# Kernel tuning notes

Measured on AMD Instinct MI355X. Metric: run time of the kernel, lower is better.

The kernel has to match this reference:

```python
import jax, jax.numpy as jnp
import numpy as np

B_, L_, V = 256, 256, 44
DM, DI, DS, DR, NL = 256, 512, 16, 16, 6  # d_model, d_inner, d_state, dt_rank, n_layers
MLP_H = 128


def setup_inputs():
    key = jax.random.key(0)
    ks = jax.random.split(key, 16)
    def nrm(i, shape, s=0.02):
        return jax.random.normal(ks[i], shape, jnp.float32) * s
    tok = jax.random.randint(ks[0], (B_, L_), 0, V, dtype=jnp.int32)
    mask = jax.random.randint(ks[1], (B_, L_), 0, 2, dtype=jnp.int32)
    emb = nrm(2, (V, 64), 0.02)
    emb = emb.at[0].set(0.0)  # padding_idx=0
    conv_w = nrm(3, (DM, 64, 3), 0.05)
    bn_gamma = jnp.ones((DM,), jnp.float32)
    bn_beta = jnp.zeros((DM,), jnp.float32)
    in_proj_w = nrm(4, (NL, 2 * DI, DM))
    conv1d_w = nrm(5, (NL, DI, 4), 0.2)
    conv1d_b = jnp.zeros((NL, DI), jnp.float32)
    x_proj_w = nrm(6, (NL, DR + 2 * DS, DI))
    dt_proj_w = nrm(7, (NL, DI, DR), 0.1)
    dt_proj_b = -4.0 + nrm(8, (NL, DI), 0.5)
    A_log = jnp.log(jnp.arange(1, DS + 1, dtype=jnp.float32))[None, None, :] * jnp.ones((NL, DI, 1), jnp.float32)
    Dp = jnp.ones((NL, DI), jnp.float32)
    out_proj_w = nrm(9, (NL, DM, DI))
    norm1_w = jnp.ones((NL, DM), jnp.float32)
    norm2_w = jnp.ones((NL, DM), jnp.float32)
    fc1_w = nrm(10, (NL, 2 * MLP_H, DM))
    fc2_w = nrm(11, (NL, DM, MLP_H))
    normf_w = jnp.ones((DM,), jnp.float32)
    normf_b = jnp.zeros((DM,), jnp.float32)
    bind_w = nrm(12, (3, DM))
    bind_b = jnp.zeros((3,), jnp.float32)
    return {"smiles_token_id": tok, "smiles_token_mask": mask, "emb": emb, "conv_w": conv_w,
            "bn_gamma": bn_gamma, "bn_beta": bn_beta, "in_proj_w": in_proj_w, "conv1d_w": conv1d_w,
            "conv1d_b": conv1d_b, "x_proj_w": x_proj_w, "dt_proj_w": dt_proj_w, "dt_proj_b": dt_proj_b,
            "A_log": A_log, "Dp": Dp, "out_proj_w": out_proj_w, "norm1_w": norm1_w, "norm2_w": norm2_w,
            "fc1_w": fc1_w, "fc2_w": fc2_w, "normf_w": normf_w, "normf_b": normf_b,
            "bind_w": bind_w, "bind_b": bind_b}


def rmsnorm(x, w, eps=1e-4):
    return x * jax.lax.rsqrt(jnp.mean(x * x, -1, keepdims=True) + eps) * w


def layernorm(x, w, b, eps=1e-4):
    mu = jnp.mean(x, -1, keepdims=True)
    var = jnp.mean((x - mu) ** 2, -1, keepdims=True)
    return (x - mu) * jax.lax.rsqrt(var + eps) * w + b


def mamba1(x, inw, cw, cb, xpw, dtw, dtb, Alog, D, outw):
    # x: [B,L,DM]
    B, L, _ = x.shape
    xz = x @ inw.T                                   # [B,L,2*DI]
    xi, z = jnp.split(xz, 2, axis=-1)
    # depthwise causal conv1d, kernel 4 (torch pads 3 then truncates to L)
    xp = jnp.pad(xi, ((0, 0), (3, 0), (0, 0)))
    xc = cb + sum(cw[:, k] * xp[:, k:k + L, :] for k in range(4))
    xc = jax.nn.silu(xc)                             # [B,L,DI]
    xdbl = xc @ xpw.T                                # [B,L,DR+2*DS]
    dt = xdbl[..., :DR]
    Bm = xdbl[..., DR:DR + DS]                       # [B,L,DS]
    Cm = xdbl[..., DR + DS:]
    dt = jax.nn.softplus(dt @ dtw.T + dtb)           # [B,L,DI]
    A = -jnp.exp(Alog)                               # [DI,DS]

    def step(h, inp):
        dt_t, u_t, B_t, C_t = inp                    # [B,DI],[B,DI],[B,DS],[B,DS]
        dA = jnp.exp(dt_t[:, :, None] * A)           # [B,DI,DS]
        h = dA * h + (dt_t * u_t)[:, :, None] * B_t[:, None, :]
        y = jnp.einsum('bdn,bn->bd', h, C_t)
        return h, y

    h0 = jnp.zeros((B, DI, DS), x.dtype)
    xs = (dt.transpose(1, 0, 2), xc.transpose(1, 0, 2), Bm.transpose(1, 0, 2), Cm.transpose(1, 0, 2))
    _, ys = jax.lax.scan(step, h0, xs)               # [L,B,DI]
    y = ys.transpose(1, 0, 2) + xc * D
    y = y * jax.nn.silu(z)
    return y @ outw.T                                # [B,L,DM]


def _forward(tok, mask, emb, conv_w, bn_gamma, bn_beta, in_proj_w, conv1d_w, conv1d_b,
             x_proj_w, dt_proj_w, dt_proj_b, A_log, Dp, out_proj_w, norm1_w, norm2_w,
             fc1_w, fc2_w, normf_w, normf_b, bind_w, bind_b):
    B, L = tok.shape
    x = emb[tok]                                     # [B,L,64]
    # conv embedding 64->256, k=3, pad=1 + BN(eval: mean 0, var 1, eps=1e-3) + relu
    xp = jnp.pad(x, ((0, 0), (1, 0 + 1), (0, 0)))
    y = sum(jnp.einsum('bli,oi->blo', xp[:, k:k + L, :], conv_w[:, :, k]) for k in range(3))
    y = y * (bn_gamma * jax.lax.rsqrt(jnp.float32(1.0 + 1e-3))) + bn_beta
    hidden = jax.nn.relu(y)                          # [B,L,DM]
    residual = None
    for i in range(NL):
        residual = hidden if residual is None else hidden + residual
        hs = rmsnorm(residual, norm1_w[i])
        hs = mamba1(hs, in_proj_w[i], conv1d_w[i], conv1d_b[i], x_proj_w[i],
                    dt_proj_w[i], dt_proj_b[i], A_log[i], Dp[i], out_proj_w[i])
        residual = hs + residual
        hs = rmsnorm(residual, norm2_w[i])
        yg = hs @ fc1_w[i].T                          # [B,L,2*MLP_H]
        y_, g = jnp.split(yg, 2, axis=-1)
        hidden = (y_ * jax.nn.silu(g)) @ fc2_w[i].T   # GatedMLP
        # dropout p=0.1 is identity in eval
    zf = layernorm(hidden + residual, normf_w, normf_b)
    m = mask[..., None].astype(jnp.float32)
    pool = (zf * m).sum(1) / m.sum(1)
    bind = pool @ bind_w.T + bind_b
    return jax.nn.sigmoid(bind)                       # [B,3]


def reference(smiles_token_id, smiles_token_mask, emb, conv_w, bn_gamma, bn_beta, in_proj_w,
              conv1d_w, conv1d_b, x_proj_w, dt_proj_w, dt_proj_b, A_log, Dp, out_proj_w,
              norm1_w, norm2_w, fc1_w, fc2_w, normf_w, normf_b, bind_w, bind_b):
    return _forward(smiles_token_id, smiles_token_mask, emb, conv_w, bn_gamma, bn_beta,
                    in_proj_w, conv1d_w, conv1d_b, x_proj_w, dt_proj_w, dt_proj_b, A_log, Dp,
                    out_proj_w, norm1_w, norm2_w, fc1_w, fc2_w, normf_w, normf_b, bind_w, bind_b)
```

## Files before the change

kernel.cpp:

```cpp
#include <hip/hip_runtime.h>
#include <math.h>

#define B_TOT 256
#define L_SEQ 256
#define DM 256
#define DI 512
#define DS 16
#define NL 6
#define MLPH 128
#define ED 64

typedef unsigned short u16;
typedef unsigned int   u32;
using bf16x8 = __attribute__((ext_vector_type(8))) short;
using f32x4  = __attribute__((ext_vector_type(4))) float;

__device__ __forceinline__ float f_sigmoid(float x){ return 1.f/(1.f+__expf(-x)); }
__device__ __forceinline__ float f_silu(float x){ return x/(1.f+__expf(-x)); }
__device__ __forceinline__ u16 f2bf(float x){
  union { float f; u32 u; } v; v.f = x;
  u32 r = v.u + 0x7fffu + ((v.u >> 16) & 1u);
  return (u16)(r >> 16);
}
__device__ __forceinline__ float bf2f(u16 h){
  union { u32 u; float f; } v; v.u = ((u32)h) << 16; return v.f;
}
__device__ __forceinline__ void pow16(float p, float* pw){
  pw[0]=p; pw[1]=p*p; pw[2]=pw[0]*pw[1]; pw[3]=pw[1]*pw[1];
  pw[4]=pw[0]*pw[3]; pw[5]=pw[1]*pw[3]; pw[6]=pw[2]*pw[3]; pw[7]=pw[3]*pw[3];
  #pragma unroll
  for(int i=0;i<8;i++) pw[8+i]=pw[7]*pw[i];
}

__global__ __launch_bounds__(256) void k_cvt(const float* __restrict__ s, u16* __restrict__ d, int n){
  int i = blockIdx.x*256 + threadIdx.x;
  if (i < n) d[i] = f2bf(s[i]);
}
__global__ __launch_bounds__(256) void k_cvt_xproj(const float* __restrict__ s, u16* __restrict__ d){
  int i = blockIdx.x*256 + threadIdx.x;
  int k = i & 511; int n = (i>>9) & 63; int l = i >> 15;
  d[i] = (n < 48) ? f2bf(s[((size_t)l*48 + n)*512 + k]) : (u16)0;
}

__global__ __launch_bounds__(256) void k_embed_conv(
    const int* __restrict__ tok, const float* __restrict__ emb,
    const float* __restrict__ cw, const float* __restrict__ gamma,
    const float* __restrict__ beta, float* __restrict__ out)
{
  const int b  = blockIdx.y;
  const int lt = blockIdx.x;
  const int tid = threadIdx.x;
  __shared__ float xs[18][ED];
  for (int idx = tid; idx < 18*ED; idx += 256){
    int t = idx / ED, i = idx - t*ED;
    int l = lt*16 + t - 1;
    float v = 0.f;
    if (l >= 0 && l < L_SEQ) v = emb[tok[b*L_SEQ + l]*ED + i];
    xs[t][i] = v;
  }
  __syncthreads();
  const float g  = gamma[tid] * rsqrtf(1.001f);
  const float bt = beta[tid];
  const float* w = cw + (size_t)tid*(ED*3);
  float acc[16];
  #pragma unroll
  for (int t=0;t<16;t++) acc[t]=0.f;
  for (int i=0;i<ED;i++){
    float w0 = w[i*3+0], w1 = w[i*3+1], w2 = w[i*3+2];
    #pragma unroll
    for (int t=0;t<16;t++)
      acc[t] += xs[t][i]*w0 + xs[t+1][i]*w1 + xs[t+2][i]*w2;
  }
  #pragma unroll
  for (int t=0;t<16;t++){
    float v = acc[t]*g + bt;
    out[((size_t)(b*L_SEQ + lt*16 + t))*DM + tid] = fmaxf(v, 0.f);
  }
}

__global__ __launch_bounds__(256) void k_rms_first(
    const float* __restrict__ residual, const float* __restrict__ w, u16* __restrict__ out)
{
  const int row  = blockIdx.x*4 + (threadIdx.x >> 6);
  const int lane = threadIdx.x & 63;
  const size_t base = (size_t)row*DM;
  float4 v = ((const float4*)(residual + base))[lane];
  float ss = v.x*v.x + v.y*v.y + v.z*v.z + v.w*v.w;
  #pragma unroll
  for (int m=1; m<64; m<<=1) ss += __shfl_xor(ss, m);
  const float sc = rsqrtf(ss*(1.f/DM) + 1e-4f);
  float4 wv = ((const float4*)w)[lane];
  u32 p0 = f2bf(v.x*sc*wv.x) | ((u32)f2bf(v.y*sc*wv.y) << 16);
  u32 p1 = f2bf(v.z*sc*wv.z) | ((u32)f2bf(v.w*sc*wv.w) << 16);
  uint2 pk; pk.x = p0; pk.y = p1;
  *(uint2*)(out + base + lane*4) = pk;
}

__global__ __launch_bounds__(256) void k_final_ln(
    const float* __restrict__ x,
    const float* __restrict__ w, const float* __restrict__ bb, float* __restrict__ out)
{
  const int row  = blockIdx.x*4 + (threadIdx.x >> 6);
  const int lane = threadIdx.x & 63;
  const size_t base = (size_t)row*DM;
  float4 v = ((const float4*)(x + base))[lane];
  float s = v.x + v.y + v.z + v.w;
  #pragma unroll
  for (int m=1; m<64; m<<=1) s += __shfl_xor(s, m);
  const float mu = s*(1.f/DM);
  float4 c; c.x=v.x-mu; c.y=v.y-mu; c.z=v.z-mu; c.w=v.w-mu;
  float ss = c.x*c.x + c.y*c.y + c.z*c.z + c.w*c.w;
  #pragma unroll
  for (int m=1; m<64; m<<=1) ss += __shfl_xor(ss, m);
  const float sc = rsqrtf(ss*(1.f/DM) + 1e-4f);
  float4 wv = ((const float4*)w)[lane];
  float4 bv = ((const float4*)bb)[lane];
  float4 o;
  o.x = c.x*sc*wv.x + bv.x; o.y = c.y*sc*wv.y + bv.y;
  o.z = c.z*sc*wv.z + bv.z; o.w = c.w*sc*wv.w + bv.w;
  ((float4*)(out + base))[lane] = o;
}

template<int BN, bool BF16OUT>
__global__ __launch_bounds__(256) void k_gemm_bf(
    const u16* __restrict__ A, const u16* __restrict__ W,
    void* __restrict__ Cv, int Nc, int K)
{
  const int n0 = blockIdx.x * BN;
  const int m0 = blockIdx.y * 128;
  const int tid = threadIdx.x;
  const int w  = tid >> 6, l = tid & 63;
  const int wr = w >> 1, wc = w & 1;
  const int lr = l & 15, kb = l >> 4;
  constexpr int NJ = BN / 32;
  __shared__ uint4 As4[128*8];
  __shared__ uint4 Bs4[BN*8];
  f32x4 acc[4][NJ];
  #pragma unroll
  for (int i=0;i<4;i++)
    #pragma unroll
    for (int j=0;j<NJ;j++)
      acc[i][j] = (f32x4){0.f,0.f,0.f,0.f};
  const int srow = tid >> 3, schunk = tid & 7;
  for (int k0 = 0; k0 < K; k0 += 64){
    #pragma unroll
    for (int i=0;i<4;i++){
      int r = i*32 + srow;
      uint4 v = *(const uint4*)(A + (size_t)(m0 + r)*K + k0 + schunk*8);
      As4[r*8 + (schunk ^ (r & 7))] = v;
    }
    #pragma unroll
    for (int i=0;i<BN/32;i++){
      int r = i*32 + srow;
      uint4 v = *(const uint4*)(W + (size_t)(n0 + r)*K + k0 + schunk*8);
      Bs4[r*8 + (schunk ^ (r & 7))] = v;
    }
    __syncthreads();
    #pragma unroll
    for (int kk=0;kk<2;kk++){
      bf16x8 af[4], bfr[NJ];
      #pragma unroll
      for (int mi=0;mi<4;mi++){
        int r = wr*64 + mi*16 + lr;
        af[mi] = *(const bf16x8*)&As4[r*8 + ((kk*4 + kb) ^ (r & 7))];
      }
      #pragma unroll
      for (int ni=0;ni<NJ;ni++){
        int r = wc*(BN/2) + ni*16 + lr;
        bfr[ni] = *(const bf16x8*)&Bs4[r*8 + ((kk*4 + kb) ^ (r & 7))];
      }
      #pragma unroll
      for (int mi=0;mi<4;mi++)
        #pragma unroll
        for (int ni=0;ni<NJ;ni++)
          acc[mi][ni] = __builtin_amdgcn_mfma_f32_16x16x32_bf16(af[mi], bfr[ni], acc[mi][ni], 0, 0, 0);
    }
    __syncthreads();
  }
  #pragma unroll
  for (int mi=0;mi<4;mi++){
    #pragma unroll
    for (int ni=0;ni<NJ;ni++){
      int col = n0 + wc*(BN/2) + ni*16 + lr;
      if (col < Nc){
        #pragma unroll
        for (int r=0;r<4;r++){
          size_t row = (size_t)(m0 + wr*64 + mi*16 + kb*4 + r);
          if (BF16OUT) ((u16*)Cv)[row*Nc + col] = f2bf(acc[mi][ni][r]);
          else         ((float*)Cv)[row*Nc + col] = acc[mi][ni][r];
        }
      }
    }
  }
}

template<bool WRITE_HS>
__global__ __launch_bounds__(512) void k_gemm_rms(
    const u16* __restrict__ A, const u16* __restrict__ W,
    float* __restrict__ residual, const float* __restrict__ nw,
    u16* __restrict__ hs, int K)
{
  const int m0 = blockIdx.x * 128;
  const int tid = threadIdx.x;
  const int w = tid >> 6, l = tid & 63;
  const int wr = w >> 1, wc = w & 1;
  const int lr = l & 15, kb = l >> 4;
  __shared__ uint4 As4[128*8];
  __shared__ uint4 Bs4[256*8];
  __shared__ float red[128][2];
  f32x4 acc[2][8];
  #pragma unroll
  for (int i=0;i<2;i++)
    #pragma unroll
    for (int j=0;j<8;j++) acc[i][j] = (f32x4){0.f,0.f,0.f,0.f};
  const int srow = tid >> 3, schunk = tid & 7;
  for (int k0 = 0; k0 < K; k0 += 64){
    #pragma unroll
    for (int i=0;i<2;i++){
      int r = i*64 + srow;
      uint4 v = *(const uint4*)(A + (size_t)(m0 + r)*K + k0 + schunk*8);
      As4[r*8 + (schunk ^ (r & 7))] = v;
    }
    #pragma unroll
    for (int i=0;i<4;i++){
      int r = i*64 + srow;
      uint4 v = *(const uint4*)(W + (size_t)r*K + k0 + schunk*8);
      Bs4[r*8 + (schunk ^ (r & 7))] = v;
    }
    __syncthreads();
    #pragma unroll
    for (int kk=0;kk<2;kk++){
      bf16x8 af[2], bfr[8];
      #pragma unroll
      for (int mi=0;mi<2;mi++){
        int r = wr*32 + mi*16 + lr;
        af[mi] = *(const bf16x8*)&As4[r*8 + ((kk*4 + kb) ^ (r & 7))];
      }
      #pragma unroll
      for (int ni=0;ni<8;ni++){
        int r = wc*128 + ni*16 + lr;
        bfr[ni] = *(const bf16x8*)&Bs4[r*8 + ((kk*4 + kb) ^ (r & 7))];
      }
      #pragma unroll
      for (int mi=0;mi<2;mi++)
        #pragma unroll
        for (int ni=0;ni<8;ni++)
          acc[mi][ni] = __builtin_amdgcn_mfma_f32_16x16x32_bf16(af[mi], bfr[ni], acc[mi][ni], 0, 0, 0);
    }
    __syncthreads();
  }
  float p[2][4];
  #pragma unroll
  for (int mi=0;mi<2;mi++)
    #pragma unroll
    for (int r=0;r<4;r++) p[mi][r] = 0.f;
  #pragma unroll
  for (int mi=0;mi<2;mi++){
    #pragma unroll
    for (int ni=0;ni<8;ni++){
      int col = wc*128 + ni*16 + lr;
      #pragma unroll
      for (int r=0;r<4;r++){
        int row = wr*32 + mi*16 + kb*4 + r;
        float v = acc[mi][ni][r] + residual[(size_t)(m0+row)*DM + col];
        acc[mi][ni][r] = v;
        p[mi][r] += v*v;
      }
    }
  }
  #pragma unroll
  for (int mi=0;mi<2;mi++)
    #pragma unroll
    for (int r=0;r<4;r++){
      float s = p[mi][r];
      s += __shfl_xor(s, 1); s += __shfl_xor(s, 2);
      s += __shfl_xor(s, 4); s += __shfl_xor(s, 8);
      p[mi][r] = s;
    }
  if (lr == 0){
    #pragma unroll
    for (int mi=0;mi<2;mi++)
      #pragma unroll
      for (int r=0;r<4;r++)
        red[wr*32 + mi*16 + kb*4 + r][wc] = p[mi][r];
  }
  __syncthreads();
  #pragma unroll
  for (int mi=0;mi<2;mi++){
    float scm[4];
    #pragma unroll
    for (int r=0;r<4;r++){
      int row = wr*32 + mi*16 + kb*4 + r;
      scm[r] = rsqrtf((red[row][0]+red[row][1])*(1.f/DM) + 1e-4f);
    }
    #pragma unroll
    for (int ni=0;ni<8;ni++){
      int col = wc*128 + ni*16 + lr;
      float wn = WRITE_HS ? nw[col] : 0.f;
      #pragma unroll
      for (int r=0;r<4;r++){
        int row = wr*32 + mi*16 + kb*4 + r;
        float v = acc[mi][ni][r];
        residual[(size_t)(m0+row)*DM + col] = v;
        if (WRITE_HS) hs[(size_t)(m0+row)*DM + col] = f2bf(v*scm[r]*wn);
      }
    }
  }
}

__global__ __launch_bounds__(512) void k_fc1_glu(
    const u16* __restrict__ A, const u16* __restrict__ W, u16* __restrict__ out)
{
  const int K = DM;
  const int m0 = blockIdx.x * 128;
  const int tid = threadIdx.x;
  const int w = tid >> 6, l = tid & 63;
  const int wr = w >> 1, wc = w & 1;
  const int lr = l & 15, kb = l >> 4;
  __shared__ uint4 As4[128*8];
  __shared__ uint4 Bs4[256*8];
  f32x4 acc[2][8];
  #pragma unroll
  for (int i=0;i<2;i++)
    #pragma unroll
    for (int j=0;j<8;j++) acc[i][j] = (f32x4){0.f,0.f,0.f,0.f};
  const int srow = tid >> 3, schunk = tid & 7;
  for (int k0 = 0; k0 < K; k0 += 64){
    #pragma unroll
    for (int i=0;i<2;i++){
      int r = i*64 + srow;
      uint4 v = *(const uint4*)(A + (size_t)(m0 + r)*K + k0 + schunk*8);
      As4[r*8 + (schunk ^ (r & 7))] = v;
    }
    #pragma unroll
    for (int i=0;i<4;i++){
      int r = i*64 + srow;
      uint4 v = *(const uint4*)(W + (size_t)r*K + k0 + schunk*8);
      Bs4[r*8 + (schunk ^ (r & 7))] = v;
    }
    __syncthreads();
    #pragma unroll
    for (int kk=0;kk<2;kk++){
      bf16x8 af[2], bfr[8];
      #pragma unroll
      for (int mi=0;mi<2;mi++){
        int r = wr*32 + mi*16 + lr;
        af[mi] = *(const bf16x8*)&As4[r*8 + ((kk*4 + kb) ^ (r & 7))];
      }
      #pragma unroll
      for (int ni=0;ni<8;ni++){
        int r = (ni < 4) ? (wc*64 + ni*16 + lr) : (128 + wc*64 + (ni-4)*16 + lr);
        bfr[ni] = *(const bf16x8*)&Bs4[r*8 + ((kk*4 + kb) ^ (r & 7))];
      }
      #pragma unroll
      for (int mi=0;mi<2;mi++)
        #pragma unroll
        for (int ni=0;ni<8;ni++)
          acc[mi][ni] = __builtin_amdgcn_mfma_f32_16x16x32_bf16(af[mi], bfr[ni], acc[mi][ni], 0, 0, 0);
    }
    __syncthreads();
  }
  #pragma unroll
  for (int mi=0;mi<2;mi++){
    #pragma unroll
    for (int ni=0;ni<4;ni++){
      int jcol = wc*64 + ni*16 + lr;
      #pragma unroll
      for (int r=0;r<4;r++){
        int row = wr*32 + mi*16 + kb*4 + r;
        float y = acc[mi][ni][r];
        float g = acc[mi][ni+4][r];
        out[(size_t)(m0+row)*MLPH + jcol] = f2bf(y * f_silu(g));
      }
    }
  }
}

__global__ __launch_bounds__(256) void k_conv1d_silu(
    const u16* __restrict__ xz, const float* __restrict__ cw,
    const float* __restrict__ cb, u16* __restrict__ xcb)
{
  const int idx = blockIdx.x*256 + threadIdx.x;
  const int d0 = (idx & 63) * 8;
  const int m  = idx >> 6;
  const int l  = m & (L_SEQ-1);
  float acc[8];
  #pragma unroll
  for (int j=0;j<8;j++) acc[j] = cb[d0+j];
  float4 wv[8];
  #pragma unroll
  for (int j=0;j<8;j++) wv[j] = *(const float4*)(cw + (d0+j)*4);
  #pragma unroll
  for (int t=0;t<4;t++){
    if (l >= 3-t){
      bf16x8 v = *(const bf16x8*)(xz + (size_t)(m-3+t)*1024 + d0);
      #pragma unroll
      for (int j=0;j<8;j++){
        float wj = (t==0)?wv[j].x:(t==1)?wv[j].y:(t==2)?wv[j].z:wv[j].w;
        acc[j] += wj * bf2f((u16)v[j]);
      }
    }
  }
  u16 o[8];
  #pragma unroll
  for (int j=0;j<8;j++) o[j] = f2bf(f_silu(acc[j]));
  *(uint4*)(xcb + (size_t)m*DI + d0) = *(uint4*)o;
}

__global__ __launch_bounds__(512) void k_scan2(
    const float* __restrict__ xdbl, const u16* __restrict__ xcb,
    const u16* __restrict__ xz, u16* __restrict__ ybf,
    const float* __restrict__ A_log, const float* __restrict__ Dp,
    const float* __restrict__ dtw, const float* __restrict__ dtb)
{
  const int b = blockIdx.x;
  const int lane = threadIdx.x & 63;
  const int w = threadIdx.x >> 6;
  const int d = blockIdx.y*64 + lane;
  __shared__ __align__(16) float BD[L_SEQ][48];
  __shared__ __align__(16) float HE[8][64][20];
  __shared__ float SD[8][64];
  const size_t rowbase = (size_t)b*L_SEQ;
  {
    const float4* src = (const float4*)(xdbl + rowbase*48);
    float4* dst = (float4*)&BD[0][0];
    #pragma unroll
    for (int j=0;j<6;j++) dst[threadIdx.x + j*512] = src[threadIdx.x + j*512];
  }
  float dtw_r[16];
  #pragma unroll
  for (int k=0;k<16;k++) dtw_r[k] = dtw[(size_t)d*16 + k];
  const float dtb_r = dtb[d];
  bool structured = true;
  #pragma unroll
  for (int n=0;n<16;n++){
    float Ar = -__expf(A_log[(size_t)d*16 + n]);
    structured = structured && (fabsf(Ar + (float)(n+1)) < 1e-4f*(float)(n+1));
  }
  const float Dv = Dp[d];
  const int l0 = w*32;
  float u_cur[8], z_cur[8];
  #pragma unroll
  for (int s=0;s<8;s++){
    u_cur[s] = bf2f(xcb[(rowbase+l0+s)*DI + d]);
    z_cur[s] = bf2f(xz [(rowbase+l0+s)*1024 + 512 + d]);
  }
  __syncthreads();
  float h[16];
  #pragma unroll
  for (int n=0;n<16;n++) h[n]=0.f;
  float cum = 0.f;
  float cumdt[32], silz[32];
  #pragma unroll
  for (int t8=0; t8<4; ++t8){
    float u_nxt[8], z_nxt[8];
    if (t8 < 3){
      #pragma unroll
      for (int s=0;s<8;s++){
        u_nxt[s] = bf2f(xcb[(rowbase+l0+t8*8+8+s)*DI + d]);
        z_nxt[s] = bf2f(xz [(rowbase+l0+t8*8+8+s)*1024 + 512 + d]);
      }
    }
    #pragma unroll
    for (int s=0;s<8;s++){
      const int i = t8*8 + s;
      const int l = l0 + i;
      const float u_v = u_cur[s], z_v = z_cur[s];
      const float4* bd4 = (const float4*)&BD[l][0];
      float4 x0=bd4[0], x1=bd4[1], x2=bd4[2], x3=bd4[3];
      float4 B0=bd4[4], B1=bd4[5], B2=bd4[6], B3=bd4[7];
      float4 C0=bd4[8], C1=bd4[9], C2=bd4[10], C3=bd4[11];
      float a0 = x0.x*dtw_r[0] + x1.x*dtw_r[4] + x2.x*dtw_r[8]  + x3.x*dtw_r[12];
      float a1 = x0.y*dtw_r[1] + x1.y*dtw_r[5] + x2.y*dtw_r[9]  + x3.y*dtw_r[13];
      float a2 = x0.z*dtw_r[2] + x1.z*dtw_r[6] + x2.z*dtw_r[10] + x3.z*dtw_r[14];
      float a3 = x0.w*dtw_r[3] + x1.w*dtw_r[7] + x2.w*dtw_r[11] + x3.w*dtw_r[15];
      const float xr = dtb_r + (a0+a1) + (a2+a3);
      const float ex = __expf(xr);
      const float dt_v = (xr > 20.f) ? xr : __logf(1.f + ex);
      cum += dt_v; cumdt[i] = cum;
      const float dtu = dt_v * u_v;
      float Bv[16] = {B0.x,B0.y,B0.z,B0.w,B1.x,B1.y,B1.z,B1.w,
                      B2.x,B2.y,B2.z,B2.w,B3.x,B3.y,B3.z,B3.w};
      float Cv[16] = {C0.x,C0.y,C0.z,C0.w,C1.x,C1.y,C1.z,C1.w,
                      C2.x,C2.y,C2.z,C2.w,C3.x,C3.y,C3.z,C3.w};
      float y0=0.f,y1=0.f,y2=0.f,y3=0.f;
      if (structured){
        const float p = 1.f/(1.f + ex);
        float pw[16]; pow16(p, pw);
        #pragma unroll
        for (int n=0;n<16;n++){
          h[n] = pw[n]*h[n] + dtu*Bv[n];
          float t = h[n]*Cv[n];
          if ((n&3)==0) y0 += t; else if ((n&3)==1) y1 += t;
          else if ((n&3)==2) y2 += t; else y3 += t;
        }
      } else {
        #pragma unroll
        for (int n=0;n<16;n++){
          float Ar = -__expf(A_log[(size_t)d*16 + n]);
          h[n] = __expf(dt_v*Ar)*h[n] + dtu*Bv[n];
          float t = h[n]*Cv[n];
          if ((n&3)==0) y0 += t; else if ((n&3)==1) y1 += t;
          else if ((n&3)==2) y2 += t; else y3 += t;
        }
      }
      const float sz = f_silu(z_v);
      silz[i] = sz;
      ybf[(rowbase+l)*DI + d] = f2bf((((y0+y1)+(y2+y3)) + u_v*Dv) * sz);
    }
    if (t8 < 3){
      #pragma unroll
      for (int s=0;s<8;s++){ u_cur[s]=u_nxt[s]; z_cur[s]=z_nxt[s]; }
    }
  }
  SD[w][lane] = cum;
  *(float4*)&HE[w][lane][0]  = make_float4(h[0],h[1],h[2],h[3]);
  *(float4*)&HE[w][lane][4]  = make_float4(h[4],h[5],h[6],h[7]);
  *(float4*)&HE[w][lane][8]  = make_float4(h[8],h[9],h[10],h[11]);
  *(float4*)&HE[w][lane][12] = make_float4(h[12],h[13],h[14],h[15]);
  __syncthreads();
  if (w == 0) return;
  float H0[16];
  #pragma unroll
  for (int n=0;n<16;n++) H0[n]=0.f;
  for (int c=0; c<w; ++c){
    float sdt = SD[c][lane];
    float4 e0 = *(const float4*)&HE[c][lane][0];
    float4 e1 = *(const float4*)&HE[c][lane][4];
    float4 e2 = *(const float4*)&HE[c][lane][8];
    float4 e3 = *(const float4*)&HE[c][lane][12];
    float he[16] = {e0.x,e0.y,e0.z,e0.w,e1.x,e1.y,e1.z,e1.w,
                    e2.x,e2.y,e2.z,e2.w,e3.x,e3.y,e3.z,e3.w};
    if (structured){
      float q = __expf(-sdt);
      float qw[16]; pow16(q, qw);
      #pragma unroll
      for (int n=0;n<16;n++) H0[n] = H0[n]*qw[n] + he[n];
    } else {
      #pragma unroll
      for (int n=0;n<16;n++){
        float Ar = -__expf(A_log[(size_t)d*16 + n]);
        H0[n] = H0[n]*__expf(Ar*sdt) + he[n];
      }
    }
  }
  #pragma unroll
  for (int t8=0; t8<4; ++t8){
    #pragma unroll
    for (int s=0;s<8;s++){
      const int i = t8*8 + s;
      const int l = l0 + i;
      const float4* bd4 = (const float4*)&BD[l][0];
      float4 C0=bd4[8], C1=bd4[9], C2=bd4[10], C3=bd4[11];
      float Cv[16] = {C0.x,C0.y,C0.z,C0.w,C1.x,C1.y,C1.z,C1.w,
                      C2.x,C2.y,C2.z,C2.w,C3.x,C3.y,C3.z,C3.w};
      float c0=0.f,c1=0.f,c2=0.f,c3=0.f;
      if (structured){
        float q = __expf(-cumdt[i]);
        float qw[16]; pow16(q, qw);
        #pragma unroll
        for (int n=0;n<16;n++){
          float t = Cv[n]*qw[n]*H0[n];
          if ((n&3)==0) c0 += t; else if ((n&3)==1) c1 += t;
          else if ((n&3)==2) c2 += t; else c3 += t;
        }
      } else {
        #pragma unroll
        for (int n=0;n<16;n++){
          float Ar = -__expf(A_log[(size_t)d*16 + n]);
          float t = Cv[n]*__expf(Ar*cumdt[i])*H0[n];
          if ((n&3)==0) c0 += t; else if ((n&3)==1) c1 += t;
          else if ((n&3)==2) c2 += t; else c3 += t;
        }
      }
      const float corr = (c0+c1)+(c2+c3);
      const size_t off = (rowbase+l)*DI + d;
      float prev = bf2f(ybf[off]);
      ybf[off] = f2bf(prev + corr*silz[i]);
    }
  }
}

__global__ __launch_bounds__(256) void k_pool(
    const float* __restrict__ zf, const int* __restrict__ mask,
    float* __restrict__ pool, int b0)
{
  const int b = blockIdx.x;
  const int d = threadIdx.x;
  __shared__ float mrow[L_SEQ];
  for (int l = d; l < L_SEQ; l += 256) mrow[l] = (float)mask[(size_t)(b0+b)*L_SEQ + l];
  __syncthreads();
  float s = 0.f, ms = 0.f;
  for (int l=0;l<L_SEQ;l++){
    float mv = mrow[l];
    s  += mv * zf[((size_t)b*L_SEQ + l)*DM + d];
    ms += mv;
  }
  pool[(size_t)(b0+b)*DM + d] = s/ms;
}

__global__ __launch_bounds__(64) void k_bind(
    const float* __restrict__ pool, const float* __restrict__ bw,
    const float* __restrict__ bb, float* __restrict__ out)
{
  const int b = blockIdx.x;
  const int lane = threadIdx.x;
  float4 p = ((const float4*)(pool + (size_t)b*DM))[lane];
  #pragma unroll
  for (int j=0;j<3;j++){
    float4 w = ((const float4*)(bw + (size_t)j*DM))[lane];
    float s = p.x*w.x + p.y*w.y + p.z*w.z + p.w*w.w;
    #pragma unroll
    for (int m=1;m<64;m<<=1) s += __shfl_xor(s, m);
    if (lane==0) out[b*3 + j] = f_sigmoid(s + bb[j]);
  }
}

extern "C" void kernel_launch(void* const* d_in, const int* in_sizes, int n_in,
                              void* d_out, int out_size, void* d_ws, size_t ws_size,
                              hipStream_t stream)
{
  const int*   tok       = (const int*)  d_in[0];
  const int*   mask      = (const int*)  d_in[1];
  const float* emb       = (const float*)d_in[2];
  const float* conv_w    = (const float*)d_in[3];
  const float* bn_gamma  = (const float*)d_in[4];
  const float* bn_beta   = (const float*)d_in[5];
  const float* in_proj_w = (const float*)d_in[6];
  const float* conv1d_w  = (const float*)d_in[7];
  const float* conv1d_b  = (const float*)d_in[8];
  const float* x_proj_w  = (const float*)d_in[9];
  const float* dt_proj_w = (const float*)d_in[10];
  const float* dt_proj_b = (const float*)d_in[11];
  const float* A_log     = (const float*)d_in[12];
  const float* Dp        = (const float*)d_in[13];
  const float* out_proj_w= (const float*)d_in[14];
  const float* norm1_w   = (const float*)d_in[15];
  const float* norm2_w   = (const float*)d_in[16];
  const float* fc1_w     = (const float*)d_in[17];
  const float* fc2_w     = (const float*)d_in[18];
  const float* normf_w   = (const float*)d_in[19];
  const float* normf_b   = (const float*)d_in[20];
  const float* bind_w    = (const float*)d_in[21];
  const float* bind_b    = (const float*)d_in[22];
  float* outp = (float*)d_out;

  char* base = (char*)d_ws;
  size_t off = 0;
  const int NIN = NL*2*DI*DM, NOUT = NL*DM*DI, NF1 = NL*2*MLPH*DM, NF2 = NL*DM*MLPH, NXP = NL*64*DI;
  u16* w_in  = (u16*)(base + off); off += (size_t)NIN*2;
  u16* w_out = (u16*)(base + off); off += (size_t)NOUT*2;
  u16* w_f1  = (u16*)(base + off); off += (size_t)NF1*2;
  u16* w_f2  = (u16*)(base + off); off += (size_t)NF2*2;
  u16* w_xp  = (u16*)(base + off); off += (size_t)NXP*2;
  float* pool = (float*)(base + off); off += (size_t)B_TOT*DM*4;
  const size_t fixed = off;

  const size_t perRow = 1216 + 4864;
  int Bc = B_TOT;
  while (Bc > 1 && fixed + (size_t)Bc*L_SEQ*perRow > ws_size) Bc >>= 1;
  const int Mc = Bc * L_SEQ;

  float* residual = (float*)(base + off); off += (size_t)Mc*DM*4;
  float* xdbl     = (float*)(base + off); off += (size_t)Mc*48*4;
  u16*   xz       = (u16*)(base + off);   off += (size_t)Mc*1024*2;
  u16*   xcb      = (u16*)(base + off);   off += (size_t)Mc*DI*2;
  u16*   ybf      = (u16*)(base + off);   off += (size_t)Mc*DI*2;
  u16*   hsbf     = (u16*)(base + off);   off += (size_t)Mc*DM*2;
  u16*   glubf    = (u16*)(base + off);   off += (size_t)Mc*MLPH*2;
  float* zf       = (float*)xz;

  k_cvt<<<(NIN +255)/256, 256, 0, stream>>>(in_proj_w,  w_in,  NIN);
  k_cvt<<<(NOUT+255)/256, 256, 0, stream>>>(out_proj_w, w_out, NOUT);
  k_cvt<<<(NF1 +255)/256, 256, 0, stream>>>(fc1_w,      w_f1,  NF1);
  k_cvt<<<(NF2 +255)/256, 256, 0, stream>>>(fc2_w,      w_f2,  NF2);
  k_cvt_xproj<<<(NXP+255)/256, 256, 0, stream>>>(x_proj_w, w_xp);

  const int nchunks = B_TOT / Bc;
  for (int c = 0; c < nchunks; ++c){
    const int b0 = c * Bc;
    k_embed_conv<<<dim3(L_SEQ/16, Bc), 256, 0, stream>>>(
        tok + (size_t)b0*L_SEQ, emb, conv_w, bn_gamma, bn_beta, residual);
    k_rms_first<<<Mc/4, 256, 0, stream>>>(residual, norm1_w, hsbf);

    for (int i = 0; i < NL; ++i){
      const u16*  inw  = w_in  + (size_t)i*(2*DI)*DM;
      const float* cw  = conv1d_w  + (size_t)i*DI*4;
      const float* cb  = conv1d_b  + (size_t)i*DI;
      const u16*  xpw  = w_xp  + (size_t)i*64*DI;
      const float* dtw = dt_proj_w + (size_t)i*DI*16;
      const float* dtb = dt_proj_b + (size_t)i*DI;
      const float* Alg = A_log     + (size_t)i*DI*DS;
      const float* Dpt = Dp        + (size_t)i*DI;
      const u16*  outw = w_out + (size_t)i*DM*DI;
      const float* n2w = norm2_w   + (size_t)i*DM;
      const u16*  f1w  = w_f1  + (size_t)i*(2*MLPH)*DM;
      const u16*  f2w  = w_f2  + (size_t)i*DM*MLPH;

      k_gemm_bf<128,true ><<<dim3((2*DI)/128, Mc/128), 256, 0, stream>>>(hsbf, inw, xz, 2*DI, DM);
      k_conv1d_silu<<<(Mc*64)/256, 256, 0, stream>>>(xz, cw, cb, xcb);
      k_gemm_bf<64, false><<<dim3(1, Mc/128), 256, 0, stream>>>(xcb, xpw, xdbl, 48, DI);
      k_scan2<<<dim3(Bc, 8), 512, 0, stream>>>(xdbl, xcb, xz, ybf, Alg, Dpt, dtw, dtb);
      k_gemm_rms<true><<<Mc/128, 512, 0, stream>>>(ybf, outw, residual, n2w, hsbf, DI);
      k_fc1_glu<<<Mc/128, 512, 0, stream>>>(hsbf, f1w, glubf);
      if (i < NL-1)
        k_gemm_rms<true ><<<Mc/128, 512, 0, stream>>>(glubf, f2w, residual,
                                                      norm1_w + (size_t)(i+1)*DM, hsbf, MLPH);
      else
        k_gemm_rms<false><<<Mc/128, 512, 0, stream>>>(glubf, f2w, residual,
                                                      nullptr, nullptr, MLPH);
    }

    k_final_ln<<<Mc/4, 256, 0, stream>>>(residual, normf_w, normf_b, zf);
    k_pool<<<Bc, 256, 0, stream>>>(zf, mask, pool, b0);
  }
  k_bind<<<B_TOT, 64, 0, stream>>>(pool, bind_w, bind_b, outp);
}
```

Measured before the change: 4.015 ms.

## Cut scan register arrays via recompute and swizzle in_proj GEMM blocks across XCDs

The scan kernel no longer keeps 32-entry per-thread arrays of cumulative dt and silu(z). In the correction pass it recomputes dt and the decay product, and reloads z from global memory. The chunk end states move to a transposed, padded shared layout so the transfer has no bank conflicts. The in_proj GEMM gets a 1D grid remapped so that consecutive M-blocks land on the same XCD for L2 reuse. The aim is lower register pressure and better cache locality, paid for with extra exp/softplus work and extra global loads of z.

Result: no change. 4.030 ms (+0.4%).

```diff
diff --git a/kernel.cpp b/kernel.cpp
--- a/kernel.cpp
+++ b/kernel.cpp
@@ -121,13 +121,21 @@
   ((float4*)(out + base))[lane] = o;
 }
 
-template<int BN, bool BF16OUT>
+template<int BN, bool BF16OUT, bool SWIZ>
 __global__ __launch_bounds__(256) void k_gemm_bf(
     const u16* __restrict__ A, const u16* __restrict__ W,
-    void* __restrict__ Cv, int Nc, int K)
-{
-  const int n0 = blockIdx.x * BN;
-  const int m0 = blockIdx.y * 128;
+    void* __restrict__ Cv, int Nc, int K, int nmb)
+{
+  int bx, by;
+  if (SWIZ){
+    const int id = blockIdx.x;
+    const int xcd = id & 7, rem = id >> 3;
+    const int per = nmb >> 3;
+    by = xcd*per + (rem % per);
+    bx = rem / per;
+  } else { bx = blockIdx.x; by = blockIdx.y; }
+  const int n0 = bx * BN;
+  const int m0 = by * 128;
   const int tid = threadIdx.x;
   const int w  = tid >> 6, l = tid & 63;
   const int wr = w >> 1, wc = w & 1;
@@ -407,7 +415,7 @@
   *(uint4*)(xcb + (size_t)m*DI + d0) = *(uint4*)o;
 }
 
-__global__ __launch_bounds__(512) void k_scan2(
+__global__ __launch_bounds__(512) void k_scan3(
     const float* __restrict__ xdbl, const u16* __restrict__ xcb,
     const u16* __restrict__ xz, u16* __restrict__ ybf,
     const float* __restrict__ A_log, const float* __restrict__ Dp,
@@ -418,7 +426,7 @@
   const int w = threadIdx.x >> 6;
   const int d = blockIdx.y*64 + lane;
   __shared__ __align__(16) float BD[L_SEQ][48];
-  __shared__ __align__(16) float HE[8][64][20];
+  __shared__ float HT[8][16][65];
   __shared__ float SD[8][64];
   const size_t rowbase = (size_t)b*L_SEQ;
   {
@@ -450,7 +458,6 @@
   #pragma unroll
   for (int n=0;n<16;n++) h[n]=0.f;
   float cum = 0.f;
-  float cumdt[32], silz[32];
   #pragma unroll
   for (int t8=0; t8<4; ++t8){
     float u_nxt[8], z_nxt[8];
@@ -463,8 +470,7 @@
     }
     #pragma unroll
     for (int s=0;s<8;s++){
-      const int i = t8*8 + s;
-      const int l = l0 + i;
+      const int l = l0 + t8*8 + s;
       const float u_v = u_cur[s], z_v = z_cur[s];
       const float4* bd4 = (const float4*)&BD[l][0];
       float4 x0=bd4[0], x1=bd4[1], x2=bd4[2], x3=bd4[3];
@@ -477,7 +483,7 @@
       const float xr = dtb_r + (a0+a1) + (a2+a3);
       const float ex = __expf(xr);
       const float dt_v = (xr > 20.f) ? xr : __logf(1.f + ex);
-      cum += dt_v; cumdt[i] = cum;
+      cum += dt_v;
       const float dtu = dt_v * u_v;
       float Bv[16] = {B0.x,B0.y,B0.z,B0.w,B1.x,B1.y,B1.z,B1.w,
                       B2.x,B2.y,B2.z,B2.w,B3.x,B3.y,B3.z,B3.w};
@@ -505,7 +511,6 @@
         }
       }
       const float sz = f_silu(z_v);
-      silz[i] = sz;
       ybf[(rowbase+l)*DI + d] = f2bf((((y0+y1)+(y2+y3)) + u_v*Dv) * sz);
     }
     if (t8 < 3){
@@ -514,10 +519,8 @@
     }
   }
   SD[w][lane] = cum;
-  *(float4*)&HE[w][lane][0]  = make_float4(h[0],h[1],h[2],h[3]);
-  *(float4*)&HE[w][lane][4]  = make_float4(h[4],h[5],h[6],h[7]);
-  *(float4*)&HE[w][lane][8]  = make_float4(h[8],h[9],h[10],h[11]);
-  *(float4*)&HE[w][lane][12] = make_float4(h[12],h[13],h[14],h[15]);
+  #pragma unroll
+  for (int n=0;n<16;n++) HT[w][n][lane] = h[n];
   __syncthreads();
   if (w == 0) return;
   float H0[16];
@@ -525,38 +528,50 @@
   for (int n=0;n<16;n++) H0[n]=0.f;
   for (int c=0; c<w; ++c){
     float sdt = SD[c][lane];
-    float4 e0 = *(const float4*)&HE[c][lane][0];
-    float4 e1 = *(const float4*)&HE[c][lane][4];
-    float4 e2 = *(const float4*)&HE[c][lane][8];
-    float4 e3 = *(const float4*)&HE[c][lane][12];
-    float he[16] = {e0.x,e0.y,e0.z,e0.w,e1.x,e1.y,e1.z,e1.w,
-                    e2.x,e2.y,e2.z,e2.w,e3.x,e3.y,e3.z,e3.w};
     if (structured){
       float q = __expf(-sdt);
       float qw[16]; pow16(q, qw);
       #pragma unroll
-      for (int n=0;n<16;n++) H0[n] = H0[n]*qw[n] + he[n];
+      for (int n=0;n<16;n++) H0[n] = H0[n]*qw[n] + HT[c][n][lane];
     } else {
       #pragma unroll
       for (int n=0;n<16;n++){
         float Ar = -__expf(A_log[(size_t)d*16 + n]);
-        H0[n] = H0[n]*__expf(Ar*sdt) + he[n];
-      }
-    }
-  }
+        H0[n] = H0[n]*__expf(Ar*sdt) + HT[c][n][lane];
+      }
+    }
+  }
+  float q = 1.f;
+  float cum2 = 0.f;
+  #pragma unroll
+  for (int s=0;s<8;s++)
+    z_cur[s] = bf2f(xz[(rowbase+l0+s)*1024 + 512 + d]);
   #pragma unroll
   for (int t8=0; t8<4; ++t8){
+    float z_nxt[8];
+    if (t8 < 3){
+      #pragma unroll
+      for (int s=0;s<8;s++)
+        z_nxt[s] = bf2f(xz[(rowbase+l0+t8*8+8+s)*1024 + 512 + d]);
+    }
     #pragma unroll
     for (int s=0;s<8;s++){
-      const int i = t8*8 + s;
-      const int l = l0 + i;
+      const int l = l0 + t8*8 + s;
       const float4* bd4 = (const float4*)&BD[l][0];
+      float4 x0=bd4[0], x1=bd4[1], x2=bd4[2], x3=bd4[3];
       float4 C0=bd4[8], C1=bd4[9], C2=bd4[10], C3=bd4[11];
+      float a0 = x0.x*dtw_r[0] + x1.x*dtw_r[4] + x2.x*dtw_r[8]  + x3.x*dtw_r[12];
+      float a1 = x0.y*dtw_r[1] + x1.y*dtw_r[5] + x2.y*dtw_r[9]  + x3.y*dtw_r[13];
+      float a2 = x0.z*dtw_r[2] + x1.z*dtw_r[6] + x2.z*dtw_r[10] + x3.z*dtw_r[14];
+      float a3 = x0.w*dtw_r[3] + x1.w*dtw_r[7] + x2.w*dtw_r[11] + x3.w*dtw_r[15];
+      const float xr = dtb_r + (a0+a1) + (a2+a3);
+      const float ex = __expf(xr);
       float Cv[16] = {C0.x,C0.y,C0.z,C0.w,C1.x,C1.y,C1.z,C1.w,
                       C2.x,C2.y,C2.z,C2.w,C3.x,C3.y,C3.z,C3.w};
       float c0=0.f,c1=0.f,c2=0.f,c3=0.f;
       if (structured){
-        float q = __expf(-cumdt[i]);
+        const float p = 1.f/(1.f + ex);
+        q *= p;
         float qw[16]; pow16(q, qw);
         #pragma unroll
         for (int n=0;n<16;n++){
@@ -565,18 +580,24 @@
           else if ((n&3)==2) c2 += t; else c3 += t;
         }
       } else {
+        const float dt_v = (xr > 20.f) ? xr : __logf(1.f + ex);
+        cum2 += dt_v;
         #pragma unroll
         for (int n=0;n<16;n++){
           float Ar = -__expf(A_log[(size_t)d*16 + n]);
-          float t = Cv[n]*__expf(Ar*cumdt[i])*H0[n];
+          float t = Cv[n]*__expf(Ar*cum2)*H0[n];
           if ((n&3)==0) c0 += t; else if ((n&3)==1) c1 += t;
           else if ((n&3)==2) c2 += t; else c3 += t;
         }
       }
-      const float corr = (c0+c1)+(c2+c3);
+      const float sz = f_silu(z_cur[s]);
       const size_t off = (rowbase+l)*DI + d;
       float prev = bf2f(ybf[off]);
-      ybf[off] = f2bf(prev + corr*silz[i]);
+      ybf[off] = f2bf(prev + ((c0+c1)+(c2+c3))*sz);
+    }
+    if (t8 < 3){
+      #pragma unroll
+      for (int s=0;s<8;s++) z_cur[s] = z_nxt[s];
     }
   }
 }
@@ -676,6 +697,8 @@
   k_cvt<<<(NF2 +255)/256, 256, 0, stream>>>(fc2_w,      w_f2,  NF2);
   k_cvt_xproj<<<(NXP+255)/256, 256, 0, stream>>>(x_proj_w, w_xp);
 
+  const int nmb = Mc/128;
+  const bool canSwiz = (nmb & 7) == 0;
   const int nchunks = B_TOT / Bc;
   for (int c = 0; c < nchunks; ++c){
     const int b0 = c * Bc;
@@ -697,10 +720,13 @@
       const u16*  f1w  = w_f1  + (size_t)i*(2*MLPH)*DM;
       const u16*  f2w  = w_f2  + (size_t)i*DM*MLPH;
 
-      k_gemm_bf<128,true ><<<dim3((2*DI)/128, Mc/128), 256, 0, stream>>>(hsbf, inw, xz, 2*DI, DM);
+      if (canSwiz)
+        k_gemm_bf<128,true,true ><<<dim3(8*nmb), 256, 0, stream>>>(hsbf, inw, xz, 2*DI, DM, nmb);
+      else
+        k_gemm_bf<128,true,false><<<dim3(8, nmb), 256, 0, stream>>>(hsbf, inw, xz, 2*DI, DM, nmb);
       k_conv1d_silu<<<(Mc*64)/256, 256, 0, stream>>>(xz, cw, cb, xcb);
-      k_gemm_bf<64, false><<<dim3(1, Mc/128), 256, 0, stream>>>(xcb, xpw, xdbl, 48, DI);
-      k_scan2<<<dim3(Bc, 8), 512, 0, stream>>>(xdbl, xcb, xz, ybf, Alg, Dpt, dtw, dtb);
+      k_gemm_bf<64, false,false><<<dim3(1, nmb), 256, 0, stream>>>(xcb, xpw, xdbl, 48, DI, nmb);
+      k_scan3<<<dim3(Bc, 8), 512, 0, stream>>>(xdbl, xcb, xz, ybf, Alg, Dpt, dtw, dtb);
       k_gemm_rms<true><<<Mc/128, 512, 0, stream>>>(ybf, outw, residual, n2w, hsbf, DI);
       k_fc1_glu<<<Mc/128, 512, 0, stream>>>(hsbf, f1w, glubf);
       if (i < NL-1)
```
